# Kernel optimization log

Hardware: AMD Instinct MI355X
Metric: run time of the kernel (lower is better)

The kernel has to match this reference:

```python
import jax, jax.numpy as jnp
import numpy as np

N = 10000
C = 16
AVG_DEG = 32
TAU = 1.0


def _label_propagate(adj, labels, train_mask, gumbel, iter_step, k_hop):
    # Faithful port of ContextLabel.LabelPropagate + get_label_distribution.
    m = train_mask[:, None]  # [N,1] bool
    Y = jnp.where(m, labels, jnp.zeros_like(labels))  # Y_pred init: zeros w/ train rows set
    for _ in range(iter_step):
        Y = adj @ Y                      # [N,N]@[N,C] propagation (memory-bound, C small)
        Y = jnp.where(m, labels, Y)      # masked overwrite of train rows
    if k_hop == 0:
        return Y
    # F.gumbel_softmax(Y, hard=True), tau=1: straight-through one-hot
    logits = (Y + gumbel) / TAU
    soft = jax.nn.softmax(logits, axis=-1)
    hard = jax.nn.one_hot(jnp.argmax(logits, axis=-1), C, dtype=soft.dtype)
    Y = hard + soft - jax.lax.stop_gradient(soft)
    Y = jnp.where(m, labels, Y)
    # k-hop adjacency power (loop over static k_hop-1)
    a = adj
    for _ in range(k_hop - 1):
        a = a @ adj
    # get_label_distribution: torch builds a dense [N,N,C] tensor with labels[j] at every
    # nonzero (i,j) of a, then sums over dim=1. That is exactly (a != 0).float() @ labels,
    # with no gradient through the nonzero pattern — computed without the N*N*C intermediate.
    mask = jax.lax.stop_gradient((a != 0).astype(Y.dtype))
    dist = mask @ Y  # [N,C] sum of neighbor label vectors
    dist = dist / jnp.sum(dist, axis=1, keepdims=True)
    return dist


def _make_adj(key):
    k1, k2 = jax.random.split(key)
    pattern = jax.random.uniform(k1, (N, N)) < (AVG_DEG / N)  # ~32 neighbors/row
    vals = jax.random.uniform(k2, (N, N))
    a = jnp.where(pattern, vals, 0.0).astype(jnp.float32)
    a = a.at[jnp.arange(N), jnp.arange(N)].set(1.0)  # self-loops -> no empty rows
    return a / jnp.sum(a, axis=1, keepdims=True)     # row-normalized


def setup_inputs() -> dict:
    key = jax.random.key(0)
    ka, kn, kl, km, kg1, kg2 = jax.random.split(key, 6)
    adj = _make_adj(ka)             # the (perturbed) adjacency passed to forward
    adj_norm = _make_adj(kn)        # the fixed adjacency used in __init__
    labels_int = jax.random.randint(kl, (N,), 0, C)
    labels_onehot = jax.nn.one_hot(labels_int, C, dtype=jnp.float32)
    train_mask = jax.random.uniform(km, (N,)) < 0.1
    # gumbel noise: -log(-log(U)), U clipped away from {0,1}
    def gum(k):
        u = jax.random.uniform(k, (N, C), minval=1e-6, maxval=1.0 - 1e-6)
        return -jnp.log(-jnp.log(u))
    gumbel_init = gum(kg1)
    gumbel = gum(kg2)
    # pseudo_labels = detached LabelPropagate(adj_norm, labels_onehot) from __init__
    pseudo_labels = _label_propagate(adj_norm, labels_onehot, train_mask, gumbel_init,
                                     iter_step=10, k_hop=1)
    return {"adj": adj, "labels_onehot": labels_onehot, "pseudo_labels": pseudo_labels,
            "gumbel": gumbel, "train_mask": train_mask, "iter_step": 10, "k_hop": 1}


def reference(adj, labels_onehot, pseudo_labels, gumbel, train_mask, iter_step, k_hop):
    out = _label_propagate(adj, labels_onehot, train_mask, gumbel, iter_step, k_hop)
    return jnp.mean((out - pseudo_labels) ** 2)  # F.mse_loss(..., reduction='mean')
```

## Files before the change

### kernel.cpp

```cpp
#include <hip/hip_runtime.h>

#define NN 10000
#define CC 16
#define CAP 96
#define NBLK 625

__device__ __forceinline__ bool mask_at(const void* p, int i, int mode) {
    if (mode == 0) return ((const int*)p)[i] != 0;
    if (mode == 1) return ((const unsigned char*)p)[i] != 0;
    return ((const float*)p)[i] != 0.0f;
}

__global__ __launch_bounds__(256) void build_csr(const float* __restrict__ adj,
                                                 int2* __restrict__ pack,
                                                 int* __restrict__ cnt,
                                                 const unsigned int* __restrict__ mask_words,
                                                 int* __restrict__ flag) {
    if (blockIdx.x == NN) {
        __shared__ int s_int_bad, s_flt_bad;
        if (threadIdx.x == 0) { s_int_bad = 0; s_flt_bad = 0; }
        __syncthreads();
        for (int i = threadIdx.x; i < NN / 4; i += 256) {
            unsigned w = mask_words[i];
            if (w > 1u) s_int_bad = 1;
            if (w != 0u && w != 0x3F800000u) s_flt_bad = 1;
        }
        __syncthreads();
        if (threadIdx.x == 0) {
            int mode;
            if (!s_int_bad)      mode = 0;
            else if (!s_flt_bad) mode = 2;
            else                 mode = 1;
            *flag = mode;
        }
        return;
    }
    __shared__ int lcnt;
    const int row = blockIdx.x;
    if (threadIdx.x == 0) lcnt = 0;
    __syncthreads();
    const float4* rp = (const float4*)(adj + (size_t)row * NN);
    int2* pb = pack + row * CAP;
    for (int i = threadIdx.x; i < NN / 4; i += 256) {
        float4 v = rp[i];
        int j = i * 4;
        if (v.x != 0.f) { int p = atomicAdd(&lcnt, 1); if (p < CAP) pb[p] = make_int2(j,     __float_as_int(v.x)); }
        if (v.y != 0.f) { int p = atomicAdd(&lcnt, 1); if (p < CAP) pb[p] = make_int2(j + 1, __float_as_int(v.y)); }
        if (v.z != 0.f) { int p = atomicAdd(&lcnt, 1); if (p < CAP) pb[p] = make_int2(j + 2, __float_as_int(v.z)); }
        if (v.w != 0.f) { int p = atomicAdd(&lcnt, 1); if (p < CAP) pb[p] = make_int2(j + 3, __float_as_int(v.w)); }
    }
    __syncthreads();
    if (threadIdx.x == 0) cnt[row] = (lcnt < CAP) ? lcnt : CAP;
}

__global__ __launch_bounds__(256) void spmv_first(const int2* __restrict__ pack,
                                                  const int* __restrict__ cnt,
                                                  const float* __restrict__ labels,
                                                  const void* __restrict__ tmask,
                                                  const int* __restrict__ flag,
                                                  float* __restrict__ Yout) {
    int t = blockIdx.x * 256 + threadIdx.x;
    int row = t >> 4, c = t & 15;
    int n = cnt[row];
    int mode = *flag;
    const int2* pp = pack + row * CAP;
    float acc = 0.0f;
    #pragma unroll 4
    for (int k = 0; k < n; k++) {
        int2 e = pp[k];
        float yv = mask_at(tmask, e.x, mode) ? labels[e.x * CC + c] : 0.0f;
        acc = fmaf(__int_as_float(e.y), yv, acc);
    }
    bool m = mask_at(tmask, row, mode);
    Yout[t] = m ? labels[t] : acc;
}

__global__ __launch_bounds__(256) void spmv_step(const int2* __restrict__ pack,
                                                 const int* __restrict__ cnt,
                                                 const float* __restrict__ Yin,
                                                 const float* __restrict__ labels,
                                                 const void* __restrict__ tmask,
                                                 const int* __restrict__ flag,
                                                 float* __restrict__ Yout) {
    int t = blockIdx.x * 256 + threadIdx.x;
    int row = t >> 4, c = t & 15;
    int n = cnt[row];
    const int2* pp = pack + row * CAP;
    float acc = 0.0f;
    #pragma unroll 4
    for (int k = 0; k < n; k++) {
        int2 e = pp[k];
        acc = fmaf(__int_as_float(e.y), Yin[e.x * CC + c], acc);
    }
    bool m = mask_at(tmask, row, *flag);
    Yout[t] = m ? labels[t] : acc;
}

__global__ __launch_bounds__(256) void spmv_harden(const int2* __restrict__ pack,
                                                   const int* __restrict__ cnt,
                                                   const float* __restrict__ Yin,
                                                   const float* __restrict__ labels,
                                                   const float* __restrict__ gumbel,
                                                   const void* __restrict__ tmask,
                                                   const int* __restrict__ flag,
                                                   float* __restrict__ Yout) {
    int t = blockIdx.x * 256 + threadIdx.x;
    int row = t >> 4, c = t & 15;
    int n = cnt[row];
    const int2* pp = pack + row * CAP;
    float acc = 0.0f;
    #pragma unroll 4
    for (int k = 0; k < n; k++) {
        int2 e = pp[k];
        acc = fmaf(__int_as_float(e.y), Yin[e.x * CC + c], acc);
    }
    bool m = mask_at(tmask, row, *flag);
    float lbl = labels[t];
    float y10 = m ? lbl : acc;
    float l = y10 + gumbel[t];
    float mx = l;
    for (int off = 8; off >= 1; off >>= 1) mx = fmaxf(mx, __shfl_xor(mx, off, 16));
    float e = expf(l - mx);
    float s = e;
    for (int off = 8; off >= 1; off >>= 1) s += __shfl_xor(s, off, 16);
    float soft = e / s;
    float hard = (l == mx) ? 1.0f : 0.0f;
    float y = (hard + soft) - soft;
    Yout[t] = m ? lbl : y;
}

__global__ __launch_bounds__(256) void mask_spmv_loss(const int2* __restrict__ pack,
                                                      const int* __restrict__ cnt,
                                                      const float* __restrict__ Y2,
                                                      const float* __restrict__ pseudo,
                                                      float* __restrict__ partial) {
    int t = blockIdx.x * 256 + threadIdx.x;
    int row = t >> 4, c = t & 15;
    int n = cnt[row];
    const int2* pp = pack + row * CAP;
    float acc = 0.0f;
    #pragma unroll 4
    for (int k = 0; k < n; k++) acc += Y2[pp[k].x * CC + c];
    float rs = acc;
    for (int off = 8; off >= 1; off >>= 1) rs += __shfl_xor(rs, off, 16);
    float d = acc / rs - pseudo[t];
    float contrib = d * d * (1.0f / (NN * CC));
    for (int off = 32; off >= 1; off >>= 1) contrib += __shfl_down(contrib, off, 64);
    __shared__ float sw[4];
    if ((threadIdx.x & 63) == 0) sw[threadIdx.x >> 6] = contrib;
    __syncthreads();
    if (threadIdx.x == 0) partial[blockIdx.x] = sw[0] + sw[1] + sw[2] + sw[3];
}

__global__ void final_reduce(const float* __restrict__ partial, float* __restrict__ out) {
    float s = 0.0f;
    for (int i = threadIdx.x; i < NBLK; i += 256) s += partial[i];
    for (int off = 32; off >= 1; off >>= 1) s += __shfl_down(s, off, 64);
    __shared__ float sw[4];
    if ((threadIdx.x & 63) == 0) sw[threadIdx.x >> 6] = s;
    __syncthreads();
    if (threadIdx.x == 0) out[0] = sw[0] + sw[1] + sw[2] + sw[3];
}

extern "C" void kernel_launch(void* const* d_in, const int* in_sizes, int n_in,
                              void* d_out, int out_size, void* d_ws, size_t ws_size,
                              hipStream_t stream) {
    const float* adj    = (const float*)d_in[0];
    const float* labels = (const float*)d_in[1];
    const float* pseudo = (const float*)d_in[2];
    const float* gumbel = (const float*)d_in[3];
    const void*  tmask  = d_in[4];

    char* ws = (char*)d_ws;
    int*   flag    = (int*)(ws + 0);
    int*   cnt     = (int*)(ws + 64);
    int2*  pack    = (int2*)(ws + 40064);
    float* Ya      = (float*)(ws + 7720064);
    float* Yb      = (float*)(ws + 8360064);
    float* partial = (float*)(ws + 9000064);

    float* outp = (float*)d_out;

    build_csr<<<NN + 1, 256, 0, stream>>>(adj, pack, cnt, (const unsigned int*)tmask, flag);

    spmv_first<<<NBLK, 256, 0, stream>>>(pack, cnt, labels, tmask, flag, Ya);
    float* cur = Ya;
    float* nxt = Yb;
    for (int it = 0; it < 8; ++it) {
        spmv_step<<<NBLK, 256, 0, stream>>>(pack, cnt, cur, labels, tmask, flag, nxt);
        float* tmp = cur; cur = nxt; nxt = tmp;
    }
    spmv_harden<<<NBLK, 256, 0, stream>>>(pack, cnt, cur, labels, gumbel, tmask, flag, nxt);
    mask_spmv_loss<<<NBLK, 256, 0, stream>>>(pack, cnt, nxt, pseudo, partial);
    final_reduce<<<1, 256, 0, stream>>>(partial, outp);
}
```

Before: 629.1 us.

## Fuse CSR build and all propagation steps into one cooperative kernel

New measurement: 1.958 ms. 211% more time.

```diff
diff --git a/kernel.cpp b/kernel.cpp
--- a/kernel.cpp
+++ b/kernel.cpp
@@ -1,14 +1,157 @@
 #include <hip/hip_runtime.h>
+#include <hip/hip_cooperative_groups.h>
+
+namespace cg = cooperative_groups;
 
 #define NN 10000
 #define CC 16
 #define CAP 96
+#define CAPP 97
+#define RPB 16
 #define NBLK 625
 
 __device__ __forceinline__ bool mask_at(const void* p, int i, int mode) {
     if (mode == 0) return ((const int*)p)[i] != 0;
     if (mode == 1) return ((const unsigned char*)p)[i] != 0;
     return ((const float*)p)[i] != 0.0f;
+}
+
+__global__ __launch_bounds__(256, 3) void fused_lp(
+        const float* __restrict__ adj,
+        const float* __restrict__ labels,
+        const float* __restrict__ pseudo,
+        const float* __restrict__ gumbel,
+        const void*  __restrict__ tmask,
+        float* __restrict__ Ya,
+        float* __restrict__ Yb,
+        float* __restrict__ partial,
+        float* __restrict__ out)
+{
+    cg::grid_group grid = cg::this_grid();
+
+    __shared__ int2 s_pack[RPB][CAPP];
+    __shared__ int  s_cnt[RPB];
+    __shared__ int  s_ib, s_fb, s_mode;
+    __shared__ float sw[4];
+
+    const int b    = blockIdx.x;
+    const int tid  = threadIdx.x;
+    const int row0 = b * RPB;
+    const int lr   = tid >> 4;
+    const int c    = tid & 15;
+    const int row  = row0 + lr;
+    const int t    = b * 256 + tid;
+
+    if (tid == 0) { s_ib = 0; s_fb = 0; }
+    if (tid < RPB) s_cnt[tid] = 0;
+    __syncthreads();
+    {
+        const unsigned int* mw = (const unsigned int*)tmask;
+        int ib = 0, fb = 0;
+        for (int i = tid; i < NN / 4; i += 256) {
+            unsigned w = mw[i];
+            ib |= (w > 1u);
+            fb |= (w != 0u && w != 0x3F800000u);
+        }
+        if (ib) s_ib = 1;
+        if (fb) s_fb = 1;
+    }
+
+    for (int idx = tid; idx < RPB * (NN / 4); idx += 256) {
+        int r = idx / (NN / 4);
+        int i = idx - r * (NN / 4);
+        float4 v = ((const float4*)(adj + (size_t)(row0 + r) * NN))[i];
+        int j = i * 4;
+        if (v.x != 0.f) { int p = atomicAdd(&s_cnt[r], 1); if (p < CAP) s_pack[r][p] = make_int2((j    ) * CC, __float_as_int(v.x)); }
+        if (v.y != 0.f) { int p = atomicAdd(&s_cnt[r], 1); if (p < CAP) s_pack[r][p] = make_int2((j + 1) * CC, __float_as_int(v.y)); }
+        if (v.z != 0.f) { int p = atomicAdd(&s_cnt[r], 1); if (p < CAP) s_pack[r][p] = make_int2((j + 2) * CC, __float_as_int(v.z)); }
+        if (v.w != 0.f) { int p = atomicAdd(&s_cnt[r], 1); if (p < CAP) s_pack[r][p] = make_int2((j + 3) * CC, __float_as_int(v.w)); }
+    }
+    if (tid == 0) s_mode = s_ib ? (s_fb ? 1 : 2) : 0;
+    __syncthreads();
+    if (tid < RPB && s_cnt[tid] > CAP) s_cnt[tid] = CAP;
+    __syncthreads();
+
+    const int  mode = s_mode;
+    const int  n    = s_cnt[lr];
+    const bool m    = mask_at(tmask, row, mode);
+    const float lbl = labels[t];
+
+    {
+        float acc = 0.f;
+        #pragma unroll 4
+        for (int k = 0; k < n; ++k) {
+            int2 e = s_pack[lr][k];
+            float yv = mask_at(tmask, e.x >> 4, mode) ? labels[e.x + c] : 0.f;
+            acc = fmaf(__int_as_float(e.y), yv, acc);
+        }
+        Ya[t] = m ? lbl : acc;
+    }
+    __threadfence();
+    grid.sync();
+
+    float* cur = Ya;
+    float* nxt = Yb;
+    for (int it = 0; it < 8; ++it) {
+        float acc = 0.f;
+        #pragma unroll 4
+        for (int k = 0; k < n; ++k) {
+            int2 e = s_pack[lr][k];
+            acc = fmaf(__int_as_float(e.y), cur[e.x + c], acc);
+        }
+        nxt[t] = m ? lbl : acc;
+        __threadfence();
+        grid.sync();
+        float* tmp = cur; cur = nxt; nxt = tmp;
+    }
+
+    {
+        float acc = 0.f;
+        #pragma unroll 4
+        for (int k = 0; k < n; ++k) {
+            int2 e = s_pack[lr][k];
+            acc = fmaf(__int_as_float(e.y), cur[e.x + c], acc);
+        }
+        float y10 = m ? lbl : acc;
+        float l = y10 + gumbel[t];
+        float mx = l;
+        for (int off = 8; off >= 1; off >>= 1) mx = fmaxf(mx, __shfl_xor(mx, off, 16));
+        float e_ = expf(l - mx);
+        float s = e_;
+        for (int off = 8; off >= 1; off >>= 1) s += __shfl_xor(s, off, 16);
+        float soft = e_ / s;
+        float hard = (l == mx) ? 1.0f : 0.0f;
+        float y = (hard + soft) - soft;
+        nxt[t] = m ? lbl : y;
+    }
+    __threadfence();
+    grid.sync();
+    const float* Y2 = nxt;
+
+    {
+        float acc = 0.f;
+        #pragma unroll 4
+        for (int k = 0; k < n; ++k) acc += Y2[s_pack[lr][k].x + c];
+        float rs = acc;
+        for (int off = 8; off >= 1; off >>= 1) rs += __shfl_xor(rs, off, 16);
+        float d = acc / rs - pseudo[t];
+        float contrib = d * d * (1.0f / (NN * CC));
+        for (int off = 32; off >= 1; off >>= 1) contrib += __shfl_down(contrib, off, 64);
+        if ((tid & 63) == 0) sw[tid >> 6] = contrib;
+        __syncthreads();
+        if (tid == 0) partial[b] = sw[0] + sw[1] + sw[2] + sw[3];
+    }
+    __threadfence();
+    grid.sync();
+
+    if (b == 0) {
+        float s = 0.f;
+        for (int i = tid; i < NBLK; i += 256) s += partial[i];
+        for (int off = 32; off >= 1; off >>= 1) s += __shfl_down(s, off, 64);
+        if ((tid & 63) == 0) sw[tid >> 6] = s;
+        __syncthreads();
+        if (tid == 0) out[0] = sw[0] + sw[1] + sw[2] + sw[3];
+    }
 }
 
 __global__ __launch_bounds__(256) void build_csr(const float* __restrict__ adj,
@@ -181,8 +324,14 @@
 
     float* outp = (float*)d_out;
 
+    void* args[] = { (void*)&adj, (void*)&labels, (void*)&pseudo, (void*)&gumbel,
+                     (void*)&tmask, (void*)&Ya, (void*)&Yb, (void*)&partial, (void*)&outp };
+    hipError_t err = hipLaunchCooperativeKernel((void*)fused_lp, dim3(NBLK), dim3(256),
+                                                args, 0, stream);
+    if (err == hipSuccess) return;
+    (void)hipGetLastError();
+
     build_csr<<<NN + 1, 256, 0, stream>>>(adj, pack, cnt, (const unsigned int*)tmask, flag);
-
     spmv_first<<<NBLK, 256, 0, stream>>>(pack, cnt, labels, tmask, flag, Ya);
     float* cur = Ya;
     float* nxt = Yb;
```

## Restructure CSR build and SpMV to use vectorized float4 gathers with interleaved packs

Applied to the files above, without the earlier changes.

Result: no change. 625.9 us (-0.5%).

```diff
diff --git a/kernel.cpp b/kernel.cpp
--- a/kernel.cpp
+++ b/kernel.cpp
@@ -3,7 +3,11 @@
 #define NN 10000
 #define CC 16
 #define CAP 96
+#define RPB 16
 #define NBLK 625
+#define CSRB 2500
+
+typedef float v4f __attribute__((ext_vector_type(4)));
 
 __device__ __forceinline__ bool mask_at(const void* p, int i, int mode) {
     if (mode == 0) return ((const int*)p)[i] != 0;
@@ -11,145 +15,223 @@
     return ((const float*)p)[i] != 0.0f;
 }
 
-__global__ __launch_bounds__(256) void build_csr(const float* __restrict__ adj,
-                                                 int2* __restrict__ pack,
-                                                 int* __restrict__ cnt,
-                                                 const unsigned int* __restrict__ mask_words,
-                                                 int* __restrict__ flag) {
-    if (blockIdx.x == NN) {
-        __shared__ int s_int_bad, s_flt_bad;
-        if (threadIdx.x == 0) { s_int_bad = 0; s_flt_bad = 0; }
+template<bool BINARY>
+static __device__ __forceinline__ v4f acc_rounds(const int4* __restrict__ pp,
+                                                 int pairs, int cg4,
+                                                 const float* __restrict__ cur) {
+    v4f a4 = {0.f, 0.f, 0.f, 0.f};
+    for (int r2 = 0; r2 < pairs; ++r2) {
+        int4 u0 = pp[4*r2], u1 = pp[4*r2+1], u2 = pp[4*r2+2], u3 = pp[4*r2+3];
+        v4f y0 = *(const v4f*)(cur + u0.x + cg4);
+        v4f y1 = *(const v4f*)(cur + u0.z + cg4);
+        v4f y2 = *(const v4f*)(cur + u1.x + cg4);
+        v4f y3 = *(const v4f*)(cur + u1.z + cg4);
+        v4f y4 = *(const v4f*)(cur + u2.x + cg4);
+        v4f y5 = *(const v4f*)(cur + u2.z + cg4);
+        v4f y6 = *(const v4f*)(cur + u3.x + cg4);
+        v4f y7 = *(const v4f*)(cur + u3.z + cg4);
+        float w0, w1, w2, w3, w4, w5, w6, w7;
+        if (BINARY) {
+            w0 = (u0.y != 0) ? 1.f : 0.f; w1 = (u0.w != 0) ? 1.f : 0.f;
+            w2 = (u1.y != 0) ? 1.f : 0.f; w3 = (u1.w != 0) ? 1.f : 0.f;
+            w4 = (u2.y != 0) ? 1.f : 0.f; w5 = (u2.w != 0) ? 1.f : 0.f;
+            w6 = (u3.y != 0) ? 1.f : 0.f; w7 = (u3.w != 0) ? 1.f : 0.f;
+        } else {
+            w0 = __int_as_float(u0.y); w1 = __int_as_float(u0.w);
+            w2 = __int_as_float(u1.y); w3 = __int_as_float(u1.w);
+            w4 = __int_as_float(u2.y); w5 = __int_as_float(u2.w);
+            w6 = __int_as_float(u3.y); w7 = __int_as_float(u3.w);
+        }
+        a4.x = fmaf(w0, y0.x, a4.x); a4.y = fmaf(w0, y0.y, a4.y); a4.z = fmaf(w0, y0.z, a4.z); a4.w = fmaf(w0, y0.w, a4.w);
+        a4.x = fmaf(w1, y1.x, a4.x); a4.y = fmaf(w1, y1.y, a4.y); a4.z = fmaf(w1, y1.z, a4.z); a4.w = fmaf(w1, y1.w, a4.w);
+        a4.x = fmaf(w2, y2.x, a4.x); a4.y = fmaf(w2, y2.y, a4.y); a4.z = fmaf(w2, y2.z, a4.z); a4.w = fmaf(w2, y2.w, a4.w);
+        a4.x = fmaf(w3, y3.x, a4.x); a4.y = fmaf(w3, y3.y, a4.y); a4.z = fmaf(w3, y3.z, a4.z); a4.w = fmaf(w3, y3.w, a4.w);
+        a4.x = fmaf(w4, y4.x, a4.x); a4.y = fmaf(w4, y4.y, a4.y); a4.z = fmaf(w4, y4.z, a4.z); a4.w = fmaf(w4, y4.w, a4.w);
+        a4.x = fmaf(w5, y5.x, a4.x); a4.y = fmaf(w5, y5.y, a4.y); a4.z = fmaf(w5, y5.z, a4.z); a4.w = fmaf(w5, y5.w, a4.w);
+        a4.x = fmaf(w6, y6.x, a4.x); a4.y = fmaf(w6, y6.y, a4.y); a4.z = fmaf(w6, y6.z, a4.z); a4.w = fmaf(w6, y6.w, a4.w);
+        a4.x = fmaf(w7, y7.x, a4.x); a4.y = fmaf(w7, y7.y, a4.y); a4.z = fmaf(w7, y7.z, a4.z); a4.w = fmaf(w7, y7.w, a4.w);
+    }
+    return a4;
+}
+
+static __device__ __forceinline__ void bfly4(v4f& v) {
+    v.x += __shfl_xor(v.x, 1, 4); v.x += __shfl_xor(v.x, 2, 4);
+    v.y += __shfl_xor(v.y, 1, 4); v.y += __shfl_xor(v.y, 2, 4);
+    v.z += __shfl_xor(v.z, 1, 4); v.z += __shfl_xor(v.z, 2, 4);
+    v.w += __shfl_xor(v.w, 1, 4); v.w += __shfl_xor(v.w, 2, 4);
+}
+
+__global__ __launch_bounds__(256) void build_csr_t(const float* __restrict__ adj,
+                                                   int2* __restrict__ pack,
+                                                   int* __restrict__ cnt,
+                                                   const unsigned int* __restrict__ mask_words,
+                                                   int* __restrict__ flag) {
+    if (blockIdx.x == CSRB) {
+        __shared__ int s_ib, s_fb;
+        if (threadIdx.x == 0) { s_ib = 0; s_fb = 0; }
         __syncthreads();
+        int ib = 0, fb = 0;
         for (int i = threadIdx.x; i < NN / 4; i += 256) {
             unsigned w = mask_words[i];
-            if (w > 1u) s_int_bad = 1;
-            if (w != 0u && w != 0x3F800000u) s_flt_bad = 1;
+            ib |= (w > 1u);
+            fb |= (w != 0u && w != 0x3F800000u);
         }
+        if (ib) s_ib = 1;
+        if (fb) s_fb = 1;
         __syncthreads();
-        if (threadIdx.x == 0) {
-            int mode;
-            if (!s_int_bad)      mode = 0;
-            else if (!s_flt_bad) mode = 2;
-            else                 mode = 1;
-            *flag = mode;
-        }
+        if (threadIdx.x == 0) *flag = s_ib ? (s_fb ? 1 : 2) : 0;
         return;
     }
-    __shared__ int lcnt;
-    const int row = blockIdx.x;
-    if (threadIdx.x == 0) lcnt = 0;
-    __syncthreads();
-    const float4* rp = (const float4*)(adj + (size_t)row * NN);
-    int2* pb = pack + row * CAP;
-    for (int i = threadIdx.x; i < NN / 4; i += 256) {
-        float4 v = rp[i];
+    __shared__ int  s_cnt[4];
+    __shared__ int2 s_p[4 * CAP];
+    const int row0 = blockIdx.x * 4;
+    for (int i = threadIdx.x; i < 4 * CAP; i += 256) s_p[i] = make_int2(0, 0);
+    if (threadIdx.x < 4) s_cnt[threadIdx.x] = 0;
+    __syncthreads();
+    for (int idx = threadIdx.x; idx < 4 * (NN / 4); idx += 256) {
+        int r = idx / (NN / 4);
+        int i = idx - r * (NN / 4);
+        float4 v = ((const float4*)(adj + (size_t)(row0 + r) * NN))[i];
         int j = i * 4;
-        if (v.x != 0.f) { int p = atomicAdd(&lcnt, 1); if (p < CAP) pb[p] = make_int2(j,     __float_as_int(v.x)); }
-        if (v.y != 0.f) { int p = atomicAdd(&lcnt, 1); if (p < CAP) pb[p] = make_int2(j + 1, __float_as_int(v.y)); }
-        if (v.z != 0.f) { int p = atomicAdd(&lcnt, 1); if (p < CAP) pb[p] = make_int2(j + 2, __float_as_int(v.z)); }
-        if (v.w != 0.f) { int p = atomicAdd(&lcnt, 1); if (p < CAP) pb[p] = make_int2(j + 3, __float_as_int(v.w)); }
-    }
-    __syncthreads();
-    if (threadIdx.x == 0) cnt[row] = (lcnt < CAP) ? lcnt : CAP;
-}
-
-__global__ __launch_bounds__(256) void spmv_first(const int2* __restrict__ pack,
-                                                  const int* __restrict__ cnt,
-                                                  const float* __restrict__ labels,
-                                                  const void* __restrict__ tmask,
-                                                  const int* __restrict__ flag,
-                                                  float* __restrict__ Yout) {
-    int t = blockIdx.x * 256 + threadIdx.x;
-    int row = t >> 4, c = t & 15;
-    int n = cnt[row];
-    int mode = *flag;
-    const int2* pp = pack + row * CAP;
-    float acc = 0.0f;
-    #pragma unroll 4
-    for (int k = 0; k < n; k++) {
-        int2 e = pp[k];
-        float yv = mask_at(tmask, e.x, mode) ? labels[e.x * CC + c] : 0.0f;
-        acc = fmaf(__int_as_float(e.y), yv, acc);
-    }
-    bool m = mask_at(tmask, row, mode);
-    Yout[t] = m ? labels[t] : acc;
-}
-
-__global__ __launch_bounds__(256) void spmv_step(const int2* __restrict__ pack,
-                                                 const int* __restrict__ cnt,
-                                                 const float* __restrict__ Yin,
-                                                 const float* __restrict__ labels,
-                                                 const void* __restrict__ tmask,
-                                                 const int* __restrict__ flag,
-                                                 float* __restrict__ Yout) {
-    int t = blockIdx.x * 256 + threadIdx.x;
-    int row = t >> 4, c = t & 15;
-    int n = cnt[row];
-    const int2* pp = pack + row * CAP;
-    float acc = 0.0f;
-    #pragma unroll 4
-    for (int k = 0; k < n; k++) {
-        int2 e = pp[k];
-        acc = fmaf(__int_as_float(e.y), Yin[e.x * CC + c], acc);
-    }
-    bool m = mask_at(tmask, row, *flag);
-    Yout[t] = m ? labels[t] : acc;
-}
-
-__global__ __launch_bounds__(256) void spmv_harden(const int2* __restrict__ pack,
+        if (v.x != 0.f) { int p = atomicAdd(&s_cnt[r], 1); if (p < CAP) s_p[r * CAP + (p & 3) * 24 + (p >> 2)] = make_int2((j    ) * CC, __float_as_int(v.x)); }
+        if (v.y != 0.f) { int p = atomicAdd(&s_cnt[r], 1); if (p < CAP) s_p[r * CAP + (p & 3) * 24 + (p >> 2)] = make_int2((j + 1) * CC, __float_as_int(v.y)); }
+        if (v.z != 0.f) { int p = atomicAdd(&s_cnt[r], 1); if (p < CAP) s_p[r * CAP + (p & 3) * 24 + (p >> 2)] = make_int2((j + 2) * CC, __float_as_int(v.z)); }
+        if (v.w != 0.f) { int p = atomicAdd(&s_cnt[r], 1); if (p < CAP) s_p[r * CAP + (p & 3) * 24 + (p >> 2)] = make_int2((j + 3) * CC, __float_as_int(v.w)); }
+    }
+    __syncthreads();
+    if (threadIdx.x < 4) cnt[row0 + threadIdx.x] = s_cnt[threadIdx.x] < CAP ? s_cnt[threadIdx.x] : CAP;
+    for (int i = threadIdx.x; i < 4 * CAP; i += 256) pack[(size_t)row0 * CAP + i] = s_p[i];
+}
+
+__global__ __launch_bounds__(256) void spmv_first_t(const int2* __restrict__ pack,
+                                                    const int* __restrict__ cnt,
+                                                    const float* __restrict__ labels,
+                                                    const void* __restrict__ tmask,
+                                                    const int* __restrict__ flag,
+                                                    float* __restrict__ Yout) {
+    const int tid = threadIdx.x;
+    const int row = blockIdx.x * RPB + (tid >> 4);
+    const int c   = tid & 15;
+    const int t   = row * CC + c;
+    const int q   = c & 3;
+    const int cg4 = c & 12;
+    const int mode = *flag;
+    const int n = cnt[row];
+    const int rounds = ((n + 15) & ~15) >> 4;
+    const int4* pp = (const int4*)(pack + (size_t)row * CAP + q * 24);
+
+    v4f a4 = {0.f, 0.f, 0.f, 0.f};
+    for (int r = 0; r < rounds; ++r) {
+        int4 u0 = pp[2 * r], u1 = pp[2 * r + 1];
+        #define ACC_LBL(ex, ew) { \
+            float w_ = __int_as_float(ew); \
+            if (w_ != 0.f && mask_at(tmask, (ex) >> 4, mode)) { \
+                v4f y_ = *(const v4f*)(labels + (ex) + cg4); \
+                a4.x = fmaf(w_, y_.x, a4.x); a4.y = fmaf(w_, y_.y, a4.y); \
+                a4.z = fmaf(w_, y_.z, a4.z); a4.w = fmaf(w_, y_.w, a4.w); } }
+        ACC_LBL(u0.x, u0.y) ACC_LBL(u0.z, u0.w) ACC_LBL(u1.x, u1.y) ACC_LBL(u1.z, u1.w)
+        #undef ACC_LBL
+    }
+    bfly4(a4);
+    if (q == 0) {
+        bool m = mask_at(tmask, row, mode);
+        v4f lbl4 = *(const v4f*)(labels + t);
+        *(v4f*)(&Yout[t]) = m ? lbl4 : a4;
+    }
+}
+
+__global__ __launch_bounds__(256) void spmv_step_t(const int2* __restrict__ pack,
                                                    const int* __restrict__ cnt,
                                                    const float* __restrict__ Yin,
                                                    const float* __restrict__ labels,
-                                                   const float* __restrict__ gumbel,
                                                    const void* __restrict__ tmask,
                                                    const int* __restrict__ flag,
                                                    float* __restrict__ Yout) {
-    int t = blockIdx.x * 256 + threadIdx.x;
-    int row = t >> 4, c = t & 15;
-    int n = cnt[row];
-    const int2* pp = pack + row * CAP;
-    float acc = 0.0f;
-    #pragma unroll 4
-    for (int k = 0; k < n; k++) {
-        int2 e = pp[k];
-        acc = fmaf(__int_as_float(e.y), Yin[e.x * CC + c], acc);
-    }
+    const int tid = threadIdx.x;
+    const int row = blockIdx.x * RPB + (tid >> 4);
+    const int c   = tid & 15;
+    const int t   = row * CC + c;
+    const int q   = c & 3;
+    const int cg4 = c & 12;
+    const int n = cnt[row];
+    const int rounds = ((n + 15) & ~15) >> 4;
+    const int pairs  = (rounds + 1) >> 1;
+    const int4* pp = (const int4*)(pack + (size_t)row * CAP + q * 24);
+
+    v4f a4 = acc_rounds<false>(pp, pairs, cg4, Yin);
+    bfly4(a4);
+    if (q == 0) {
+        bool m = mask_at(tmask, row, *flag);
+        v4f lbl4 = *(const v4f*)(labels + t);
+        *(v4f*)(&Yout[t]) = m ? lbl4 : a4;
+    }
+}
+
+__global__ __launch_bounds__(256) void spmv_harden_t(const int2* __restrict__ pack,
+                                                     const int* __restrict__ cnt,
+                                                     const float* __restrict__ Yin,
+                                                     const float* __restrict__ labels,
+                                                     const float* __restrict__ gumbel,
+                                                     const void* __restrict__ tmask,
+                                                     const int* __restrict__ flag,
+                                                     float* __restrict__ Yout) {
+    const int tid = threadIdx.x;
+    const int row = blockIdx.x * RPB + (tid >> 4);
+    const int c   = tid & 15;
+    const int t   = row * CC + c;
+    const int q   = c & 3;
+    const int cg4 = c & 12;
+    const int n = cnt[row];
+    const int rounds = ((n + 15) & ~15) >> 4;
+    const int pairs  = (rounds + 1) >> 1;
+    const int4* pp = (const int4*)(pack + (size_t)row * CAP + q * 24);
+
+    v4f a4 = acc_rounds<false>(pp, pairs, cg4, Yin);
+    bfly4(a4);
+    float acc = (q == 0) ? a4.x : (q == 1) ? a4.y : (q == 2) ? a4.z : a4.w;
     bool m = mask_at(tmask, row, *flag);
     float lbl = labels[t];
     float y10 = m ? lbl : acc;
     float l = y10 + gumbel[t];
     float mx = l;
     for (int off = 8; off >= 1; off >>= 1) mx = fmaxf(mx, __shfl_xor(mx, off, 16));
-    float e = expf(l - mx);
-    float s = e;
+    float e_ = expf(l - mx);
+    float s = e_;
     for (int off = 8; off >= 1; off >>= 1) s += __shfl_xor(s, off, 16);
-    float soft = e / s;
+    float soft = e_ / s;
     float hard = (l == mx) ? 1.0f : 0.0f;
     float y = (hard + soft) - soft;
     Yout[t] = m ? lbl : y;
 }
 
-__global__ __launch_bounds__(256) void mask_spmv_loss(const int2* __restrict__ pack,
-                                                      const int* __restrict__ cnt,
-                                                      const float* __restrict__ Y2,
-                                                      const float* __restrict__ pseudo,
-                                                      float* __restrict__ partial) {
-    int t = blockIdx.x * 256 + threadIdx.x;
-    int row = t >> 4, c = t & 15;
-    int n = cnt[row];
-    const int2* pp = pack + row * CAP;
-    float acc = 0.0f;
-    #pragma unroll 4
-    for (int k = 0; k < n; k++) acc += Y2[pp[k].x * CC + c];
+__global__ __launch_bounds__(256) void mask_loss_t(const int2* __restrict__ pack,
+                                                   const int* __restrict__ cnt,
+                                                   const float* __restrict__ Y2,
+                                                   const float* __restrict__ pseudo,
+                                                   float* __restrict__ partial) {
+    const int tid = threadIdx.x;
+    const int row = blockIdx.x * RPB + (tid >> 4);
+    const int c   = tid & 15;
+    const int t   = row * CC + c;
+    const int q   = c & 3;
+    const int cg4 = c & 12;
+    const int n = cnt[row];
+    const int rounds = ((n + 15) & ~15) >> 4;
+    const int pairs  = (rounds + 1) >> 1;
+    const int4* pp = (const int4*)(pack + (size_t)row * CAP + q * 24);
+
+    v4f a4 = acc_rounds<true>(pp, pairs, cg4, Y2);
+    bfly4(a4);
+    float acc = (q == 0) ? a4.x : (q == 1) ? a4.y : (q == 2) ? a4.z : a4.w;
     float rs = acc;
     for (int off = 8; off >= 1; off >>= 1) rs += __shfl_xor(rs, off, 16);
     float d = acc / rs - pseudo[t];
     float contrib = d * d * (1.0f / (NN * CC));
     for (int off = 32; off >= 1; off >>= 1) contrib += __shfl_down(contrib, off, 64);
     __shared__ float sw[4];
-    if ((threadIdx.x & 63) == 0) sw[threadIdx.x >> 6] = contrib;
-    __syncthreads();
-    if (threadIdx.x == 0) partial[blockIdx.x] = sw[0] + sw[1] + sw[2] + sw[3];
+    if ((tid & 63) == 0) sw[tid >> 6] = contrib;
+    __syncthreads();
+    if (tid == 0) partial[blockIdx.x] = sw[0] + sw[1] + sw[2] + sw[3];
 }
 
 __global__ void final_reduce(const float* __restrict__ partial, float* __restrict__ out) {
@@ -181,16 +263,16 @@
 
     float* outp = (float*)d_out;
 
-    build_csr<<<NN + 1, 256, 0, stream>>>(adj, pack, cnt, (const unsigned int*)tmask, flag);
-
-    spmv_first<<<NBLK, 256, 0, stream>>>(pack, cnt, labels, tmask, flag, Ya);
+    build_csr_t<<<CSRB + 1, 256, 0, stream>>>(adj, pack, cnt,
+                                              (const unsigned int*)tmask, flag);
+    spmv_first_t<<<NBLK, 256, 0, stream>>>(pack, cnt, labels, tmask, flag, Ya);
     float* cur = Ya;
     float* nxt = Yb;
     for (int it = 0; it < 8; ++it) {
-        spmv_step<<<NBLK, 256, 0, stream>>>(pack, cnt, cur, labels, tmask, flag, nxt);
+        spmv_step_t<<<NBLK, 256, 0, stream>>>(pack, cnt, cur, labels, tmask, flag, nxt);
         float* tmp = cur; cur = nxt; nxt = tmp;
     }
-    spmv_harden<<<NBLK, 256, 0, stream>>>(pack, cnt, cur, labels, gumbel, tmask, flag, nxt);
-    mask_spmv_loss<<<NBLK, 256, 0, stream>>>(pack, cnt, nxt, pseudo, partial);
+    spmv_harden_t<<<NBLK, 256, 0, stream>>>(pack, cnt, cur, labels, gumbel, tmask, flag, nxt);
+    mask_loss_t<<<NBLK, 256, 0, stream>>>(pack, cnt, nxt, pseudo, partial);
     final_reduce<<<1, 256, 0, stream>>>(partial, outp);
 }
```
